# Kernel optimization log

Hardware: AMD Instinct MI355X
Metric: run time of the kernel (lower is better)

## Reference

```python
import jax, jax.numpy as jnp
import numpy as np

# Module hyperparameters (init_kwargs)
N_CLASSES = 21
RADIUS = 5
SIZE = (256, 256)
SIGMA_DIST = 4.0
SIGMA_FEAT = 1.0
B, C = 8, 32


def _offsets(radius):
    """Integer (dy, dx) offsets with Euclidean distance < radius (includes (0,0))."""
    offs = []
    r = int(radius)
    for dy in range(-r + 1, r):
        for dx in range(-r + 1, r):
            if dy * dy + dx * dx < radius * radius:
                offs.append((dy, dx))
    return offs


OFFSETS = _offsets(RADIUS)  # 69 offsets for radius=5


def setup_inputs() -> dict:
    key = jax.random.key(0)
    k1, k2 = jax.random.split(key)
    H, W = SIZE
    classification = jax.random.uniform(k1, (B, N_CLASSES, H, W), dtype=jnp.float32)
    features = jax.random.normal(k2, (B, C, H, W), dtype=jnp.float32)
    return {"classification": classification, "features": features}


def reference(classification, features):
    # classification: [B, K, H, W] soft assignments S
    # features:       [B, C, H, W]
    Bb, K, H, W = classification.shape
    inv_sd2 = 1.0 / (SIGMA_DIST * SIGMA_DIST)
    inv_sf2 = 1.0 / (SIGMA_FEAT * SIGMA_FEAT)

    hs = jnp.arange(H)
    ws = jnp.arange(W)

    WS = jnp.zeros_like(classification)           # (W @ S), [B, K, H, W]
    degree = jnp.zeros((Bb, H, W), classification.dtype)

    # Loop over the small fixed set of neighbor offsets (69 for radius=5).
    for dy, dx in OFFSETS:
        f_nb = jnp.roll(features, (-dy, -dx), axis=(2, 3))
        s_nb = jnp.roll(classification, (-dy, -dx), axis=(2, 3))
        # mask out wrap-around: neighbor (h+dy, w+dx) must be in-bounds
        valid_h = (hs + dy >= 0) & (hs + dy < H)
        valid_w = (ws + dx >= 0) & (ws + dx < W)
        mask = (valid_h[:, None] & valid_w[None, :]).astype(classification.dtype)
        # Gaussian affinity: distance kernel * feature kernel
        feat_d2 = ((features - f_nb) ** 2).sum(axis=1)        # [B, H, W]
        w = jnp.exp(-(dy * dy + dx * dx) * inv_sd2 - feat_d2 * inv_sf2) * mask
        WS = WS + w[:, None] * s_nb
        degree = degree + w

    # numerator   = S^T W S : [B, K, K]
    # denominator = d^T S   : [B, K]
    num = jnp.einsum('bkhw,bjhw->bkj', classification, WS)
    den = jnp.einsum('bhw,bkhw->bk', degree, classification)
    return (num / den[:, None, :]).sum()
```

## Files before the change

kernel.cpp:

```cpp
#include <hip/hip_runtime.h>

#define HH 256
#define WW 256
#define HWPX 65536
#define BB 8
#define KK 21
#define CC 32
#define NOUT (BB * KK)
#define AFF_BLOCKS 1024

typedef _Float16 half2v __attribute__((ext_vector_type(2)));
union F4H { float4 f4; half2v h[4]; };

__global__ __launch_bounds__(256) void prep(const float* __restrict__ cls,
                                            const float* __restrict__ feat,
                                            float4* __restrict__ fpk,
                                            float2* __restrict__ TN,
                                            float* __restrict__ accum ) {
    if (blockIdx.x == 0) {
        for (int i = threadIdx.x; i < NOUT * 2 + 1; i += 256)
            ((unsigned*)accum)[i] = 0u;
    }

    const int tid = blockIdx.x * 256 + threadIdx.x;
    const int b = tid >> 16;
    const int p = tid & (HWPX - 1);

    const float* cbase = cls + (size_t)b * KK * HWPX + p;
    float s = 0.f;
#pragma unroll
    for (int k = 0; k < KK; ++k) s += cbase[(size_t)k * HWPX];

    const float* src = feat + (size_t)b * CC * HWPX + p;
    float nq = 0.f;
#pragma unroll 1
    for (int j = 0; j < 4; ++j) {
        float ch[8];
#pragma unroll
        for (int c = 0; c < 8; ++c) ch[c] = src[(size_t)(j * 8 + c) * HWPX];
        F4H u;
#pragma unroll
        for (int k = 0; k < 4; ++k) {
            u.h[k] = __builtin_bit_cast(half2v, __builtin_amdgcn_cvt_pkrtz(ch[2 * k], ch[2 * k + 1]));
            nq = __builtin_amdgcn_fdot2(u.h[k], u.h[k], nq, false);
        }
        fpk[(size_t)j * (BB * HWPX) + tid] = u.f4;
    }
    TN[tid] = make_float2(s, nq);
}

__global__ __launch_bounds__(256) void affinity6(const float4* __restrict__ fpk,
                                                 const float2* __restrict__ TN,
                                                 const float* __restrict__ cls,
                                                 float* __restrict__ numer,
                                                 float* __restrict__ denom,
                                                 unsigned* __restrict__ counter,
                                                 float* __restrict__ out) {
    __shared__ float smV[1024], smD[1024];
    __shared__ float pN[4][22], pD[4][22];
    __shared__ float sm[4];
    __shared__ unsigned sdone;

    const int L    = blockIdx.x;
    const int b    = L & 7;
    const int rest = L >> 3;
    const int half = rest & 1;
    const int t    = rest >> 1;
    const int by   = t & 15;
    const int bx   = t >> 4;
    const int lane = threadIdx.x & 63;
    const int wid  = threadIdx.x >> 6;
    const int gx   = bx * 64 + lane;
    const int gy0  = by * 16 + wid * 4;

    const size_t bofs = (size_t)b * HWPX;
    const float4* fb0 = fpk + bofs;
    const float4* fb1 = fpk + (size_t)1 * BB * HWPX + bofs;
    const float4* fb2 = fpk + (size_t)2 * BB * HWPX + bofs;
    const float4* fb3 = fpk + (size_t)3 * BB * HWPX + bofs;
    const float2* tnb = TN + bofs;

    F4H fp[4][4];
    float np_[4];
#pragma unroll
    for (int py = 0; py < 4; ++py) {
        const int pp = ((gy0 + py) << 8) | gx;
        fp[py][0].f4 = fb0[pp];
        fp[py][1].f4 = fb1[pp];
        fp[py][2].f4 = fb2[pp];
        fp[py][3].f4 = fb3[pp];
        np_[py] = tnb[pp].y;
    }

    float degacc[4] = {0.f, 0.f, 0.f, 0.f};
    float vacc[4]   = {0.f, 0.f, 0.f, 0.f};

    const int dy_lo = half * 6;
    const int dy_hi = dy_lo + 6;

#pragma unroll 1
    for (int dyi = dy_lo; dyi < dy_hi; ++dyi) {
        const int ny = gy0 + dyi - 4;
        if ((unsigned)ny >= HH) continue;
        const int rowq = ny << 8;

        int dy2[4];
        float base[4];
#pragma unroll
        for (int py = 0; py < 4; ++py) {
            const int d = dyi - 4 - py;
            dy2[py] = d * d;
            base[py] = fmaf(-0.03125f, (float)dy2[py], -0.5f * np_[py]);
        }
        const int mind = min(min(dy2[0], dy2[1]), min(dy2[2], dy2[3]));

#pragma unroll 3
        for (int dxi = 0; dxi < 9; ++dxi) {
            const int dx = dxi - 4;
            const int dx2 = dx * dx;
            if (mind + dx2 >= 25) continue;

            const int gx2 = gx + dx;
            const bool vx = (unsigned)gx2 < WW;
            const int q = rowq | min(max(gx2, 0), WW - 1);

            F4H nb0, nb1, nb2, nb3;
            nb0.f4 = fb0[q];
            nb1.f4 = fb1[q];
            nb2.f4 = fb2[q];
            nb3.f4 = fb3[q];
            const float2 tq = tnb[q];
            const float cdx = (float)dx2 * -0.03125f;

#pragma unroll
            for (int py = 0; py < 4; ++py) {
                if (dy2[py] + dx2 < 25) {
                    float acc = fmaf(-0.5f, tq.y, base[py] + cdx);
#pragma unroll
                    for (int k = 0; k < 4; ++k) {
                        acc = __builtin_amdgcn_fdot2(fp[py][0].h[k], nb0.h[k], acc, false);
                        acc = __builtin_amdgcn_fdot2(fp[py][1].h[k], nb1.h[k], acc, false);
                        acc = __builtin_amdgcn_fdot2(fp[py][2].h[k], nb2.h[k], acc, false);
                        acc = __builtin_amdgcn_fdot2(fp[py][3].h[k], nb3.h[k], acc, false);
                    }
                    float w = __builtin_exp2f(acc * 2.8853900817779268f);
                    w = vx ? w : 0.f;
                    degacc[py] += w;
                    vacc[py] = fmaf(w, tq.x, vacc[py]);
                }
            }
        }
    }

#pragma unroll
    for (int py = 0; py < 4; ++py) {
        const int li = ((wid * 4 + py) << 6) | lane;
        smV[li] = vacc[py];
        smD[li] = degacc[py];
    }
    __syncthreads();

    const int li0 = threadIdx.x * 4;
    const int lr  = li0 >> 6;
    const int lc  = li0 & 63;
    const int gp  = ((by * 16 + lr) << 8) | (bx * 64 + lc);
    const float4 v4 = *(const float4*)&smV[li0];
    const float4 d4 = *(const float4*)&smD[li0];
    const float* clsb = cls + (size_t)b * KK * HWPX + gp;

    float accN[KK], accD[KK];
#pragma unroll 7
    for (int j = 0; j < KK; ++j) {
        float4 s4 = *(const float4*)(clsb + (size_t)j * HWPX);
        float n = s4.x * v4.x;   n = fmaf(s4.y, v4.y, n);
        n = fmaf(s4.z, v4.z, n); n = fmaf(s4.w, v4.w, n);
        float d = s4.x * d4.x;   d = fmaf(s4.y, d4.y, d);
        d = fmaf(s4.z, d4.z, d); d = fmaf(s4.w, d4.w, d);
        accN[j] = n; accD[j] = d;
    }

#pragma unroll
    for (int j = 0; j < KK; ++j) {
        float n = accN[j], d = accD[j];
#pragma unroll
        for (int off = 32; off > 0; off >>= 1) {
            n += __shfl_down(n, off);
            d += __shfl_down(d, off);
        }
        if (lane == 0) { pN[wid][j] = n; pD[wid][j] = d; }
    }
    __syncthreads();
    if (threadIdx.x < 2 * KK) {
        int h2 = threadIdx.x / KK;
        int j = threadIdx.x - h2 * KK;
        float acc = h2 ? (pD[0][j] + pD[1][j] + pD[2][j] + pD[3][j])
                       : (pN[0][j] + pN[1][j] + pN[2][j] + pN[3][j]);
        float* dst = h2 ? denom : numer;
        atomicAdd(&dst[b * KK + j], acc);
    }

    if (threadIdx.x == 0) {
        __threadfence();
        unsigned old = atomicAdd(counter, 1u);
        sdone = (old == (unsigned)(AFF_BLOCKS - 1)) ? 1u : 0u;
    }
    __syncthreads();
    if (sdone) {
        const int i = threadIdx.x;
        float r = 0.f;
        if (i < NOUT) {
            float n = atomicAdd(&numer[i], 0.f);
            float d = atomicAdd(&denom[i], 0.f);
            r = n / d;
        }
#pragma unroll
        for (int off = 32; off > 0; off >>= 1) r += __shfl_down(r, off);
        if ((i & 63) == 0) sm[i >> 6] = r;
        __syncthreads();
        if (i == 0) out[0] = sm[0] + sm[1] + sm[2] + sm[3];
    }
}

extern "C" void kernel_launch(void* const* d_in, const int* in_sizes, int n_in,
                              void* d_out, int out_size, void* d_ws, size_t ws_size,
                              hipStream_t stream) {
    const float* cls  = (const float*)d_in[0];
    const float* feat = (const float*)d_in[1];
    float* out = (float*)d_out;

    const size_t BHW = (size_t)BB * HWPX;
    float4*   fpk     = (float4*)d_ws;
    float2*   TN      = (float2*)((char*)d_ws + BHW * 64);
    float*    numer   = (float*)((char*)TN + BHW * 8);
    float*    denom   = numer + NOUT;
    unsigned* counter = (unsigned*)(denom + NOUT);

    prep<<<dim3(BHW / 256), dim3(256), 0, stream>>>(cls, feat, fpk, TN, numer);
    affinity6<<<dim3(AFF_BLOCKS), dim3(256), 0, stream>>>(fpk, TN, cls, numer, denom, counter, out);
}
```

Measured before the change: 213.1 us.

## Vectorize prep through an LDS transpose and merge the affinity dy-halves into one block

The prep kernel now has each block handle 1024 pixels. Threads load float4 vectors of class and feature planes, pack channel pairs to fp16 and stage them in LDS, then write the per-pixel packed records and norms. This is meant to cut per-load overhead versus the earlier scalar strided loads. The affinity kernel drops its split of the dy range across two blocks, so 512 blocks each cover all 12 dy rows. That halves the redundant classification reads and atomics in the epilogue, but launches fewer blocks and exposes less parallelism on a large GPU.

Result: no change. 211.8 us (-0.6%).

```diff
diff --git a/kernel.cpp b/kernel.cpp
--- a/kernel.cpp
+++ b/kernel.cpp
@@ -7,49 +7,85 @@
 #define KK 21
 #define CC 32
 #define NOUT (BB * KK)
-#define AFF_BLOCKS 1024
+#define AFF_BLOCKS 512
 
 typedef _Float16 half2v __attribute__((ext_vector_type(2)));
 union F4H { float4 f4; half2v h[4]; };
+union U1H { unsigned u; half2v h; };
+
+__device__ __forceinline__ half2v pk(float a, float b) {
+    return __builtin_bit_cast(half2v, __builtin_amdgcn_cvt_pkrtz(a, b));
+}
 
 __global__ __launch_bounds__(256) void prep(const float* __restrict__ cls,
                                             const float* __restrict__ feat,
-                                            float4* __restrict__ fpk,
+                                            uint4* __restrict__ fpk,
                                             float2* __restrict__ TN,
-                                            float* __restrict__ accum ) {
+                                            float* __restrict__ accum) {
+    __shared__ unsigned ldsW[4][1024];
+    __shared__ float    ldsT[1024];
+
     if (blockIdx.x == 0) {
         for (int i = threadIdx.x; i < NOUT * 2 + 1; i += 256)
             ((unsigned*)accum)[i] = 0u;
     }
 
-    const int tid = blockIdx.x * 256 + threadIdx.x;
-    const int b = tid >> 16;
-    const int p = tid & (HWPX - 1);
-
-    const float* cbase = cls + (size_t)b * KK * HWPX + p;
-    float s = 0.f;
-#pragma unroll
-    for (int k = 0; k < KK; ++k) s += cbase[(size_t)k * HWPX];
-
-    const float* src = feat + (size_t)b * CC * HWPX + p;
-    float nq = 0.f;
+    const int b    = blockIdx.x >> 6;
+    const int tile = blockIdx.x & 63;
+    const int px0  = tile << 10;
+    const int t    = threadIdx.x;
+    const size_t gbase = (size_t)b * HWPX + px0;
+
+    const float* cb = cls + (size_t)b * KK * HWPX + px0 + 4 * t;
+    float4 s = make_float4(0.f, 0.f, 0.f, 0.f);
+#pragma unroll
+    for (int k = 0; k < KK; ++k) {
+        float4 c = *(const float4*)(cb + (size_t)k * HWPX);
+        s.x += c.x; s.y += c.y; s.z += c.z; s.w += c.w;
+    }
+    *(float4*)&ldsT[4 * t] = s;
+
+    const float* fb = feat + (size_t)b * CC * HWPX + px0 + 4 * t;
+    float nqacc[4] = {0.f, 0.f, 0.f, 0.f};
 #pragma unroll 1
     for (int j = 0; j < 4; ++j) {
-        float ch[8];
-#pragma unroll
-        for (int c = 0; c < 8; ++c) ch[c] = src[(size_t)(j * 8 + c) * HWPX];
-        F4H u;
-#pragma unroll
-        for (int k = 0; k < 4; ++k) {
-            u.h[k] = __builtin_bit_cast(half2v, __builtin_amdgcn_cvt_pkrtz(ch[2 * k], ch[2 * k + 1]));
-            nq = __builtin_amdgcn_fdot2(u.h[k], u.h[k], nq, false);
-        }
-        fpk[(size_t)j * (BB * HWPX) + tid] = u.f4;
-    }
-    TN[tid] = make_float2(s, nq);
-}
-
-__global__ __launch_bounds__(256) void affinity6(const float4* __restrict__ fpk,
+#pragma unroll
+        for (int cp = 0; cp < 4; ++cp) {
+            float4 a = *(const float4*)(fb + (size_t)(8 * j + 2 * cp) * HWPX);
+            float4 c = *(const float4*)(fb + (size_t)(8 * j + 2 * cp + 1) * HWPX);
+            uint4 u;
+            u.x = __builtin_bit_cast(unsigned, pk(a.x, c.x));
+            u.y = __builtin_bit_cast(unsigned, pk(a.y, c.y));
+            u.z = __builtin_bit_cast(unsigned, pk(a.z, c.z));
+            u.w = __builtin_bit_cast(unsigned, pk(a.w, c.w));
+            *(uint4*)&ldsW[cp][4 * t] = u;
+        }
+        __syncthreads();
+#pragma unroll
+        for (int r = 0; r < 4; ++r) {
+            const int lp = (r << 8) + t;
+            U1H w0, w1, w2, w3;
+            w0.u = ldsW[0][lp]; w1.u = ldsW[1][lp];
+            w2.u = ldsW[2][lp]; w3.u = ldsW[3][lp];
+            float nq = nqacc[r];
+            nq = __builtin_amdgcn_fdot2(w0.h, w0.h, nq, false);
+            nq = __builtin_amdgcn_fdot2(w1.h, w1.h, nq, false);
+            nq = __builtin_amdgcn_fdot2(w2.h, w2.h, nq, false);
+            nq = __builtin_amdgcn_fdot2(w3.h, w3.h, nq, false);
+            nqacc[r] = nq;
+            uint4 rec = make_uint4(w0.u, w1.u, w2.u, w3.u);
+            fpk[(size_t)j * (BB * HWPX) + gbase + lp] = rec;
+        }
+        __syncthreads();
+    }
+#pragma unroll
+    for (int r = 0; r < 4; ++r) {
+        const int lp = (r << 8) + t;
+        TN[gbase + lp] = make_float2(ldsT[lp], nqacc[r]);
+    }
+}
+
+__global__ __launch_bounds__(256) void affinity5(const float4* __restrict__ fpk,
                                                  const float2* __restrict__ TN,
                                                  const float* __restrict__ cls,
                                                  float* __restrict__ numer,
@@ -61,17 +97,15 @@
     __shared__ float sm[4];
     __shared__ unsigned sdone;
 
-    const int L    = blockIdx.x;
-    const int b    = L & 7;
-    const int rest = L >> 3;
-    const int half = rest & 1;
-    const int t    = rest >> 1;
-    const int by   = t & 15;
-    const int bx   = t >> 4;
+    const int L  = blockIdx.x;
+    const int b  = L & 7;
+    const int t  = L >> 3;
+    const int by = t & 15;
+    const int bx = t >> 4;
     const int lane = threadIdx.x & 63;
     const int wid  = threadIdx.x >> 6;
-    const int gx   = bx * 64 + lane;
-    const int gy0  = by * 16 + wid * 4;
+    const int gx  = bx * 64 + lane;
+    const int gy0 = by * 16 + wid * 4;
 
     const size_t bofs = (size_t)b * HWPX;
     const float4* fb0 = fpk + bofs;
@@ -95,11 +129,8 @@
     float degacc[4] = {0.f, 0.f, 0.f, 0.f};
     float vacc[4]   = {0.f, 0.f, 0.f, 0.f};
 
-    const int dy_lo = half * 6;
-    const int dy_hi = dy_lo + 6;
-
 #pragma unroll 1
-    for (int dyi = dy_lo; dyi < dy_hi; ++dyi) {
+    for (int dyi = 0; dyi < 12; ++dyi) {
         const int ny = gy0 + dyi - 4;
         if ((unsigned)ny >= HH) continue;
         const int rowq = ny << 8;
@@ -229,12 +260,13 @@
     float* out = (float*)d_out;
 
     const size_t BHW = (size_t)BB * HWPX;
-    float4*   fpk     = (float4*)d_ws;
+    uint4*    fpk     = (uint4*)d_ws;
     float2*   TN      = (float2*)((char*)d_ws + BHW * 64);
     float*    numer   = (float*)((char*)TN + BHW * 8);
     float*    denom   = numer + NOUT;
     unsigned* counter = (unsigned*)(denom + NOUT);
 
-    prep<<<dim3(BHW / 256), dim3(256), 0, stream>>>(cls, feat, fpk, TN, numer);
-    affinity6<<<dim3(AFF_BLOCKS), dim3(256), 0, stream>>>(fpk, TN, cls, numer, denom, counter, out);
-}
+    prep<<<dim3(512), dim3(256), 0, stream>>>(cls, feat, fpk, TN, numer);
+    affinity5<<<dim3(AFF_BLOCKS), dim3(256), 0, stream>>>((const float4*)fpk, TN, cls,
+                                                          numer, denom, counter, out);
+}
```
